# Kernel tuning notes

Measured on AMD Instinct MI355X. Metric: run time of the kernel, lower is better.

The kernel has to match this reference:

```python
import jax, jax.numpy as jnp
import numpy as np

B = 64        # BATCH_SIZE
C_IN = 16
L = 8192
FFT0 = 64
FFT1 = 256
CO = 32       # c_out per fft branch (c_out=64 / 2 ffts)
RATIO = FFT1 // FFT0  # 4
EPS = 1e-5


def setup_inputs() -> dict:
    key = jax.random.key(0)
    ks = jax.random.split(key, 12)
    x = jax.random.normal(ks[0], (B, C_IN, L), jnp.float32)
    bn_gamma = 1.0 + 0.1 * jax.random.normal(ks[1], (2, B), jnp.float32)
    bn_beta = 0.1 * jax.random.normal(ks[2], (2, B), jnp.float32)
    mk_r = 0.1 * jax.random.normal(ks[3], (RATIO, RATIO), jnp.float32)
    mk_i = 0.1 * jax.random.normal(ks[4], (RATIO, RATIO), jnp.float32)
    mb_r = 0.1 * jax.random.normal(ks[5], (RATIO,), jnp.float32)
    mb_i = 0.1 * jax.random.normal(ks[6], (RATIO,), jnp.float32)
    fk0_r = 0.1 * jax.random.normal(ks[7], (FFT0 // 2 + 1, C_IN, CO), jnp.float32)
    fk0_i = 0.1 * jax.random.normal(ks[8], (FFT0 // 2 + 1, C_IN, CO), jnp.float32)
    fk1_r = 0.1 * jax.random.normal(ks[9], (FFT1 // 2 + 1, C_IN, CO), jnp.float32)
    fk1_i = 0.1 * jax.random.normal(ks[10], (FFT1 // 2 + 1, C_IN, CO), jnp.float32)
    pbias = 0.1 * jax.random.normal(ks[11], (2 * CO,), jnp.float32)
    return dict(x=x, bn_gamma=bn_gamma, bn_beta=bn_beta, mk_r=mk_r, mk_i=mk_i,
                mb_r=mb_r, mb_i=mb_i, fk0_r=fk0_r, fk0_i=fk0_i,
                fk1_r=fk1_r, fk1_i=fk1_i, pbias=pbias)


def _stft(x2d, n):
    # torch.stft(center=True, pad_mode='reflect', hop=n_fft, rect window),
    # then keep onesided bins and drop the last frame (as in the module).
    N = x2d.shape[0]
    xp = jnp.pad(x2d, ((0, 0), (n // 2, n // 2)), mode='reflect')
    frames = xp.reshape(N, -1, n)               # (N, T+1, n), hop == n_fft
    spec = jnp.fft.rfft(frames, axis=-1)        # onesided == [:, :, :n//2+1]
    return spec[:, :-1, :]                      # drop last frame -> (N, T, n//2+1)


def _zero_interp(p, ratio, out_f):
    # interleave (ratio-1) zeros along the freq axis, then crop to out_f bins
    b, t, f, c = p.shape
    z = jnp.zeros((b, t, f, ratio - 1, c), p.dtype)
    q = jnp.concatenate([p[:, :, :, None, :], z], axis=3).reshape(b, t, f * ratio, c)
    return q[:, :, :out_f, :]


def _cbn(xc, g, b):
    # BatchNorm2d(BATCH_SIZE) after permute(3,0,1,2): channel dim == batch dim,
    # stats over (c_in, T, F) per batch element; complex mean, |.|^2 variance.
    mu = jnp.mean(xc, axis=(1, 2, 3), keepdims=True)
    d = xc - mu
    var = jnp.mean((d * jnp.conj(d)).real, axis=(1, 2, 3), keepdims=True)
    xh = d / jnp.sqrt(var + EPS)
    return xh * g[:, None, None, None] + b[:, None, None, None]


def _istft(out, n):
    # out: (B, T, F, CO) complex. Mirrors permute/reshape + frame repeat + istft
    # (hop=n_fft, rect window, center=True -> trim n//2 on both ends).
    Bq, T, F, Co = out.shape
    pf = out.transpose(0, 3, 2, 1).reshape(Bq * Co, F, T)
    pf = jnp.concatenate([pf, pf[:, :, :1]], axis=-1)   # append copy of frame 0 -> T+1 frames
    fr = jnp.fft.irfft(pf, n=n, axis=1)                 # (N, n, T+1)
    sig = fr.transpose(0, 2, 1).reshape(Bq * Co, -1)    # overlap-add trivial (hop=n)
    sig = sig[:, n // 2: n // 2 + T * n]                # length L
    return sig.reshape(Bq, Co, -1).transpose(0, 2, 1)   # (B, L, CO)


def _forward(x, bn_gamma, bn_beta, mk_r, mk_i, mb_r, mb_i,
             fk0_r, fk0_i, fk1_r, fk1_i, pbias):
    x2 = x.reshape(B * C_IN, L)

    def spec(n):
        s = _stft(x2, n)                                 # (B*C_IN, T, n//2+1)
        T = s.shape[1]
        return s.reshape(B, C_IN, T, n // 2 + 1).transpose(0, 2, 3, 1)  # (B,T,F,C_IN)

    p0 = spec(FFT0)   # (B, 128, 33, 16)
    p1 = spec(FFT1)   # (B, 32, 129, 16)

    # attention merge across time (small fft -> large fft scale)
    pm = p0.reshape(B, -1, RATIO, FFT0 // 2 + 1, C_IN).transpose(0, 1, 3, 4, 2)  # (B,T1,F0,C,r)
    kc = mk_r + 1j * mk_i
    att = jnp.einsum('btfcr,rs->btfcs', pm, kc) + (mb_r + 1j * mb_i)
    a = jax.nn.softmax(jnp.abs(att), axis=-1)            # real weights (complex(a,0) in torch)
    merged = jnp.sum(pm * a, axis=-1) * float(RATIO)     # (B, T1, F0, C_IN)

    F1 = FFT1 // 2 + 1
    mask01 = _zero_interp(jnp.ones(merged.shape, jnp.float32), RATIO, F1)
    up = _zero_interp(merged, RATIO, F1)

    acc0 = p0                                            # own-scale mask is all ones
    acc1 = mask01 * up + (1.0 - mask01) * p1             # cross-scale + complementary mask

    def head(acc, g, b, fkr, fki, n):
        xbn = _cbn(acc, g, b)
        out = jnp.einsum('btfi,fio->btfo', xbn, fkr + 1j * fki)  # FILTER_FLAG merge
        return _istft(out, n)

    t0 = head(acc0, bn_gamma[0], bn_beta[0], fk0_r, fk0_i, FFT0)  # (B, L, CO)
    t1 = head(acc1, bn_gamma[1], bn_beta[1], fk1_r, fk1_i, FFT1)  # (B, L, CO)

    y = jnp.concatenate([t0, t1], axis=2) + pbias        # + patch_bias.real
    y = jax.nn.relu(y)                                   # ACT_DOMAIN == 'time'
    return y.transpose(0, 2, 1)                          # (B, c_out, L)


def reference(x, bn_gamma, bn_beta, mk_r, mk_i, mb_r, mb_i,
              fk0_r, fk0_i, fk1_r, fk1_i, pbias):
    return _forward(x, bn_gamma, bn_beta, mk_r, mk_i, mb_r, mb_i,
                    fk0_r, fk0_i, fk1_r, fk1_i, pbias)
```

## Files before the change

### kernel.cpp

```cpp
#include <hip/hip_runtime.h>
#include <math.h>

#define BB   64
#define CIN  16
#define LL   8192
#define CO   32
#define TCO  64
constexpr int T0n = 128;
constexpr int T1n = 32;
constexpr int F0n = 33;
constexpr int F1n = 129;

typedef unsigned int   uint32;
typedef unsigned short u16;
typedef __attribute__((ext_vector_type(8))) _Float16 half8;
typedef __attribute__((ext_vector_type(4))) float    f32x4;
typedef __attribute__((ext_vector_type(4))) uint32   u32x4;

__device__ inline int imin(int a, int b) { return a < b ? a : b; }

__device__ inline half8 flip_pm(half8 v) {
    u32x4 u;
    __builtin_memcpy(&u, &v, 16);
    u.y ^= 0x80008000u;
    u.w ^= 0x80008000u;
    half8 r;
    __builtin_memcpy(&r, &u, 16);
    return r;
}

template<int N, int F, int TFR, int NTILES, int KTT, int MT_W, int NT_W,
         int NT_STRIDE, bool MT_SPLIT>
__global__ __launch_bounds__(256)
void stft_mfma_kernel(const float* __restrict__ x,
                      const u16* __restrict__ dhi, const u16* __restrict__ dlo,
                      float* __restrict__ p) {
    constexpr int PADN = N + 8;
    __shared__ __align__(16) u16 Xhi[TFR * PADN];
    __shared__ __align__(16) u16 Xlo[TFR * PADN];
    int bc = blockIdx.x;
    const float* xrow = x + (size_t)bc * LL;

    for (int i = threadIdx.x; i < TFR * N; i += 256) {
        int row = i / N, colk = i % N;
        int gi = i - N / 2;
        gi = gi < 0 ? -gi : gi;
        float v = xrow[gi];
        _Float16 h = (_Float16)v;
        _Float16 l = (_Float16)(v - (float)h);
        Xhi[row * PADN + colk] = *(u16*)&h;
        Xlo[row * PADN + colk] = *(u16*)&l;
    }
    __syncthreads();

    int lane = threadIdx.x & 63, w = threadIdx.x >> 6;
    int col = lane & 15, quad = lane >> 4;
    f32x4 acc[MT_W][NT_W];
    #pragma unroll
    for (int mi = 0; mi < MT_W; ++mi)
        #pragma unroll
        for (int nj = 0; nj < NT_W; ++nj) {
            f32x4 z = {0.f, 0.f, 0.f, 0.f};
            acc[mi][nj] = z;
        }

    for (int kt = 0; kt < KTT; ++kt) {
        half8 ah[MT_W], al[MT_W];
        #pragma unroll
        for (int mi = 0; mi < MT_W; ++mi) {
            int mt = MT_SPLIT ? (w * MT_W + mi) : mi;
            int t  = mt * 16 + col;
            ah[mi] = *(const half8*)&Xhi[t * PADN + kt * 32 + quad * 8];
            al[mi] = *(const half8*)&Xlo[t * PADN + kt * 32 + quad * 8];
        }
        #pragma unroll
        for (int nj = 0; nj < NT_W; ++nj) {
            int nt = MT_SPLIT ? nj : (w + nj * NT_STRIDE);
            if (nt < NTILES) {
                half8 bh = ((const half8*)dhi)[(nt * KTT + kt) * 64 + lane];
                half8 bl = ((const half8*)dlo)[(nt * KTT + kt) * 64 + lane];
                #pragma unroll
                for (int mi = 0; mi < MT_W; ++mi) {
                    acc[mi][nj] = __builtin_amdgcn_mfma_f32_16x16x32_f16(ah[mi], bh, acc[mi][nj], 0, 0, 0);
                    acc[mi][nj] = __builtin_amdgcn_mfma_f32_16x16x32_f16(ah[mi], bl, acc[mi][nj], 0, 0, 0);
                    acc[mi][nj] = __builtin_amdgcn_mfma_f32_16x16x32_f16(al[mi], bh, acc[mi][nj], 0, 0, 0);
                }
            }
        }
    }

    int b = bc / CIN, c = bc % CIN;
    #pragma unroll
    for (int mi = 0; mi < MT_W; ++mi) {
        int mt = MT_SPLIT ? (w * MT_W + mi) : mi;
        #pragma unroll
        for (int nj = 0; nj < NT_W; ++nj) {
            int nt = MT_SPLIT ? nj : (w + nj * NT_STRIDE);
            if (nt < NTILES) {
                int j = nt * 16 + col;
                if (j < 2 * F) {
                    int t0 = mt * 16 + quad * 4;
                    f32x4 a = acc[mi][nj];
                    #pragma unroll
                    for (int r = 0; r < 4; ++r) {
                        p[(((size_t)b * TFR + t0 + r) * CIN + c) * (2 * F) + j] = a[r];
                    }
                }
            }
        }
    }
}

__global__ __launch_bounds__(256)
void init_d_kernel(u16* __restrict__ dhi0, u16* __restrict__ dlo0,
                   u16* __restrict__ dhi1, u16* __restrict__ dlo1) {
    int idx = blockIdx.x * 256 + threadIdx.x;
    constexpr int SZ0 = 5 * 2 * 64 * 8;
    constexpr int SZ1 = 17 * 8 * 64 * 8;
    int N, F, KTT, id; u16 *dh, *dl;
    if (idx < SZ0)            { N = 64;  F = F0n; KTT = 2; dh = dhi0; dl = dlo0; id = idx; }
    else if (idx < SZ0 + SZ1) { N = 256; F = F1n; KTT = 8; dh = dhi1; dl = dlo1; id = idx - SZ0; }
    else return;
    int jj   = id & 7;
    int lane = (id >> 3) & 63;
    int rest = id >> 9;
    int kt   = rest % KTT;
    int nt   = rest / KTT;
    int j = nt * 16 + (lane & 15);
    int k = kt * 32 + (lane >> 4) * 8 + jj;
    float v = 0.f;
    if (j < 2 * F) {
        int f = j >> 1;
        int u = (f * k) % N;
        double th = 6.283185307179586476925286766559 * (double)u / (double)N;
        v = (float)((j & 1) ? -sin(th) : cos(th));
    }
    _Float16 h = (_Float16)v;
    _Float16 l = (_Float16)(v - (float)h);
    dh[id] = *(u16*)&h;
    dl[id] = *(u16*)&l;
}

__global__ __launch_bounds__(256)
void merge_kernel(const float2* __restrict__ p0, float2* __restrict__ p1,
                  const float* __restrict__ mkr, const float* __restrict__ mki,
                  const float* __restrict__ mbr, const float* __restrict__ mbi) {
    int idx = blockIdx.x * 256 + threadIdx.x;
    const int total = BB * T1n * CIN * F0n;
    if (idx >= total) return;
    int f0 = idx % F0n; int r1 = idx / F0n;
    int c  = r1 % CIN;  int r2 = r1 / CIN;
    int t1 = r2 % T1n;  int b  = r2 / T1n;
    float2 pm[4];
    #pragma unroll
    for (int r = 0; r < 4; ++r) {
        int t = t1 * 4 + r;
        pm[r] = p0[(((size_t)b * T0n + t) * CIN + c) * F0n + f0];
    }
    float mag[4], mx = -1e30f;
    #pragma unroll
    for (int s = 0; s < 4; ++s) {
        float atr = mbr[s], ati = mbi[s];
        #pragma unroll
        for (int r = 0; r < 4; ++r) {
            float kr = mkr[r * 4 + s], ki = mki[r * 4 + s];
            atr = fmaf(pm[r].x, kr, atr); atr = fmaf(-pm[r].y, ki, atr);
            ati = fmaf(pm[r].x, ki, ati); ati = fmaf(pm[r].y, kr, ati);
        }
        mag[s] = sqrtf(atr * atr + ati * ati);
        mx = fmaxf(mx, mag[s]);
    }
    float se = 0.f;
    #pragma unroll
    for (int s = 0; s < 4; ++s) { mag[s] = expf(mag[s] - mx); se += mag[s]; }
    float inv = 4.0f / se;
    float mr = 0.f, mi = 0.f;
    #pragma unroll
    for (int r = 0; r < 4; ++r) { mr = fmaf(pm[r].x, mag[r], mr); mi = fmaf(pm[r].y, mag[r], mi); }
    p1[(((size_t)b * T1n + t1) * CIN + c) * F1n + 4 * f0] = make_float2(mr * inv, mi * inv);
}

__global__ __launch_bounds__(256)
void cbn_partial_kernel(const float2* __restrict__ p0, const float2* __restrict__ p1,
                        float4* __restrict__ part) {
    int blk  = blockIdx.x;
    int c8   = blk & 7;
    int b    = (blk >> 3) & 63;
    int head = blk >> 9;
    int Nel  = head ? (T1n * CIN * F1n) : (T0n * CIN * F0n);
    const float2* base = head ? (p1 + (size_t)b * (T1n * CIN * F1n))
                              : (p0 + (size_t)b * (T0n * CIN * F0n));
    int chunk = (Nel + 7) / 8;
    int i0 = c8 * chunk, i1 = imin(i0 + chunk, Nel);
    float sr = 0.f, si = 0.f, s2 = 0.f;
    for (int i = i0 + threadIdx.x; i < i1; i += 256) {
        float2 v = base[i];
        sr += v.x; si += v.y;
        s2 = fmaf(v.x, v.x, s2); s2 = fmaf(v.y, v.y, s2);
    }
    __shared__ float red[3][256];
    red[0][threadIdx.x] = sr; red[1][threadIdx.x] = si; red[2][threadIdx.x] = s2;
    __syncthreads();
    for (int off = 128; off > 0; off >>= 1) {
        if (threadIdx.x < off) {
            red[0][threadIdx.x] += red[0][threadIdx.x + off];
            red[1][threadIdx.x] += red[1][threadIdx.x + off];
            red[2][threadIdx.x] += red[2][threadIdx.x + off];
        }
        __syncthreads();
    }
    if (threadIdx.x == 0)
        part[blk] = make_float4(red[0][0], red[1][0], red[2][0], 0.f);
}

__global__ __launch_bounds__(128)
void cbn_final_kernel(const float4* __restrict__ part,
                      const float* __restrict__ gamma, const float* __restrict__ beta,
                      float4* __restrict__ bn) {
    int hb = threadIdx.x;
    float sr = 0.f, si = 0.f, s2 = 0.f;
    #pragma unroll
    for (int c = 0; c < 8; ++c) {
        float4 v = part[hb * 8 + c];
        sr += v.x; si += v.y; s2 += v.z;
    }
    int head = hb >> 6;
    int Nel  = head ? (T1n * CIN * F1n) : (T0n * CIN * F0n);
    float invN = 1.f / (float)Nel;
    float mur = sr * invN, mui = si * invN;
    float var = s2 * invN - mur * mur - mui * mui;
    float g = gamma[hb] * rsqrtf(var + 1e-5f);
    bn[hb] = make_float4(g, beta[hb] - mur * g, -mui * g, 0.f);
}

__global__ __launch_bounds__(256)
void init_w_kernel(u16* __restrict__ whi0, u16* __restrict__ wlo0,
                   u16* __restrict__ whi1, u16* __restrict__ wlo1) {
    int idx = blockIdx.x * 256 + threadIdx.x;
    constexpr int SZ0 = 2 * 3 * 64 * 8;
    constexpr int SZ1 = 8 * 9 * 64 * 8;
    int N, F, KT, id; u16 *dh, *dl;
    if (idx < SZ0)            { N = 64;  F = F0n; KT = 3; dh = whi0; dl = wlo0; id = idx; }
    else if (idx < SZ0 + SZ1) { N = 256; F = F1n; KT = 9; dh = whi1; dl = wlo1; id = idx - SZ0; }
    else return;
    int j    = id & 7;
    int lane = (id >> 3) & 63;
    int rest = id >> 9;
    int kt   = rest % KT;
    int mt   = rest / KT;
    int m  = mt * 16 + (lane & 15);
    int k2 = kt * 32 + (lane >> 4) * 8 + j;
    float v = 0.f;
    if (k2 < 2 * F) {
        int f = k2 >> 1;
        double scale = (f == 0 || f == F - 1) ? (1024.0 / N) : (2048.0 / N);
        int u = (m * f) % N;
        double th = 6.283185307179586476925286766559 * (double)u / (double)N;
        v = (float)((k2 & 1) ? (-scale * sin(th)) : (scale * cos(th)));
    }
    _Float16 h = (_Float16)v;
    _Float16 l = (_Float16)(v - (float)h);
    dh[id] = *(u16*)&h;
    dl[id] = *(u16*)&l;
}

__global__ __launch_bounds__(256)
void init_fk_kernel(const float* __restrict__ r0, const float* __restrict__ i0,
                    const float* __restrict__ r1, const float* __restrict__ i1,
                    float4* __restrict__ q0, float4* __restrict__ q1,
                    float2* __restrict__ s0, float2* __restrict__ s1) {
    int idx = blockIdx.x * 256 + threadIdx.x;
    constexpr int NQ0 = 8 * F0n * 32;
    constexpr int NQ1 = 8 * F1n * 32;
    constexpr int NS0 = F0n * 32;
    constexpr int NS1 = F1n * 32;
    if (idx < NQ0) {
        int id = idx;
        int c2 = id / (F0n * 32); int rem = id % (F0n * 32);
        int o = rem / F0n, f = rem % F0n;
        int s = (f * CIN + 2 * c2) * CO + o;
        q0[id] = make_float4(r0[s], i0[s], r0[s + CO], i0[s + CO]);
    } else if (idx < NQ0 + NQ1) {
        int id = idx - NQ0;
        int c2 = id / (F1n * 32); int rem = id % (F1n * 32);
        int o = rem / F1n, f = rem % F1n;
        int s = (f * CIN + 2 * c2) * CO + o;
        q1[id] = make_float4(r1[s], i1[s], r1[s + CO], i1[s + CO]);
    } else if (idx < NQ0 + NQ1 + NS0) {
        int id = idx - NQ0 - NQ1;
        int o = id / F0n, f = id % F0n;
        float sr = 0.f, si = 0.f;
        for (int ci = 0; ci < CIN; ++ci) {
            int s = (f * CIN + ci) * CO + o;
            sr += r0[s]; si += i0[s];
        }
        s0[id] = make_float2(sr, si);
    } else if (idx < NQ0 + NQ1 + NS0 + NS1) {
        int id = idx - NQ0 - NQ1 - NS0;
        int o = id / F1n, f = id % F1n;
        float sr = 0.f, si = 0.f;
        for (int ci = 0; ci < CIN; ++ci) {
            int s = (f * CIN + ci) * CO + o;
            sr += r1[s]; si += i1[s];
        }
        s1[id] = make_float2(sr, si);
    }
}

template<int F, int TFR, int CH0, int FCH, int TCH>
__global__ __launch_bounds__(256)
void einsum_kernel(const float2* __restrict__ p, const float4* __restrict__ fkq,
                   const float2* __restrict__ fks, const float4* __restrict__ bn,
                   uint32* __restrict__ Ghi, uint32* __restrict__ Glo) {
    constexpr int FCO  = F * 32;
    constexpr int NFCH = (F + FCH - 1) / FCH;
    constexpr int NTC  = TFR / TCH;
    static_assert(FCH == 8 && TCH * CIN * FCH % 256 == 0, "cfg");
    __shared__ float2 xs[TCH][CIN][FCH];
    int blk  = blockIdx.x;
    int fch  = blk % NFCH;
    int rest = blk / NFCH;
    int tc   = rest % NTC;
    int b    = rest / NTC;
    int t0   = tc * TCH;
    int f0   = fch * FCH;
    int o    = threadIdx.x >> 3;
    int fl   = threadIdx.x & 7;
    int f    = f0 + fl;
    bool valid = f < F;
    int fc = valid ? f : F - 1;
    float4 kk[8];
    #pragma unroll
    for (int c2 = 0; c2 < 8; ++c2) kk[c2] = fkq[c2 * FCO + o * F + fc];
    float2 fv = fks[o * F + fc];
    float4 par = bn[(CH0 ? 1 : 0) * BB + b];
    float base_re = fmaf(par.y, fv.x, -par.z * fv.y);
    float base_im = fmaf(par.y, fv.y,  par.z * fv.x);

    const float2* pb = p + (size_t)(b * TFR + t0) * CIN * F;
    for (int i = threadIdx.x; i < TCH * CIN * FCH; i += 256) {
        int fi = i & 7;
        int r  = i >> 3;
        int ff = f0 + fi;
        ((float2*)xs)[i] = (ff < F) ? pb[(size_t)r * F + ff] : make_float2(0.f, 0.f);
    }
    __syncthreads();
    for (int tp = 0; tp < TCH; ++tp) {
        float re = 0.f, im = 0.f;
        #pragma unroll
        for (int c2 = 0; c2 < 8; ++c2) {
            float2 xa = xs[tp][2 * c2][fl];
            float2 xb = xs[tp][2 * c2 + 1][fl];
            float4 kkc = kk[c2];
            re = fmaf(xa.x, kkc.x, re); re = fmaf(-xa.y, kkc.y, re);
            im = fmaf(xa.x, kkc.y, im); im = fmaf(xa.y, kkc.x, im);
            re = fmaf(xb.x, kkc.z, re); re = fmaf(-xb.y, kkc.w, re);
            im = fmaf(xb.x, kkc.w, im); im = fmaf(xb.y, kkc.z, im);
        }
        if (valid) {
            float res = fmaf(par.x, re, base_re) * 32.f;
            float ims = fmaf(par.x, im, base_im) * 32.f;
            _Float16 rh = (_Float16)res; _Float16 rl = (_Float16)(res - (float)rh);
            _Float16 ih = (_Float16)ims; _Float16 il = (_Float16)(ims - (float)ih);
            size_t d = ((size_t)(b * TFR + t0 + tp) * 32 + o) * F + f;
            Ghi[d] = ((uint32)(*(u16*)&ih) << 16) | (uint32)(*(u16*)&rh);
            Glo[d] = ((uint32)(*(u16*)&il) << 16) | (uint32)(*(u16*)&rl);
        }
    }
}

template<int N, int F, int TFR, int CH0, int KT, int WMT, bool NTSPLIT>
__global__ __launch_bounds__(256)
void irfft_kernel(const uint32* __restrict__ Ghi, const uint32* __restrict__ Glo,
                  const u16* __restrict__ whi, const u16* __restrict__ wlo,
                  const float* __restrict__ pbias, float* __restrict__ out) {
    constexpr int PADW = KT * 16;
    constexpr int LDW  = PADW + 4;
    constexpr int WNT  = NTSPLIT ? 1 : 2;
    __shared__ __align__(16) uint32 buf[2][32 * LDW];
    int t  = blockIdx.x % (TFR + 1);
    int b  = blockIdx.x / (TFR + 1);
    int tf = (t == TFR) ? 0 : t;
    const uint32* sH = Ghi + (size_t)(b * TFR + tf) * 32 * F;
    const uint32* sL = Glo + (size_t)(b * TFR + tf) * 32 * F;
    for (int i = threadIdx.x; i < 32 * F; i += 256) {
        int row = i / F, c = i - row * F;
        buf[0][row * LDW + c] = sH[i];
        buf[1][row * LDW + c] = sL[i];
    }
    for (int i = threadIdx.x; i < 32 * (PADW - F); i += 256) {
        constexpr int cols = PADW - F;
        int row = i / cols, c = i - row * cols;
        buf[0][row * LDW + F + c] = 0;
        buf[1][row * LDW + F + c] = 0;
    }
    __syncthreads();

    int lane = threadIdx.x & 63, w = threadIdx.x >> 6;
    int col = lane & 15, quad = lane >> 4;
    const u16* bufh = (const u16*)&buf[0][0];
    const u16* bufl = (const u16*)&buf[1][0];

    f32x4 accB[WMT][WNT], accD[WMT][WNT];
    #pragma unroll
    for (int mi = 0; mi < WMT; ++mi)
        #pragma unroll
        for (int nj = 0; nj < WNT; ++nj) {
            f32x4 z = {0.f, 0.f, 0.f, 0.f};
            accB[mi][nj] = z; accD[mi][nj] = z;
        }
    for (int kt = 0; kt < KT; ++kt) {
        half8 bh[WNT], bl[WNT], bhm[WNT], blm[WNT];
        #pragma unroll
        for (int nj = 0; nj < WNT; ++nj) {
            int nt = NTSPLIT ? (w & 1) : nj;
            int ro = (nt * 16 + col) * (2 * LDW) + kt * 32 + quad * 8;
            bh[nj]  = *(const half8*)(bufh + ro);
            bl[nj]  = *(const half8*)(bufl + ro);
            bhm[nj] = flip_pm(bh[nj]);
            blm[nj] = flip_pm(bl[nj]);
        }
        #pragma unroll
        for (int mi = 0; mi < WMT; ++mi) {
            int mt = NTSPLIT ? (w >> 1) : (w * WMT + mi);
            half8 ah = ((const half8*)whi)[(mt * KT + kt) * 64 + lane];
            half8 al = ((const half8*)wlo)[(mt * KT + kt) * 64 + lane];
            #pragma unroll
            for (int nj = 0; nj < WNT; ++nj) {
                accB[mi][nj] = __builtin_amdgcn_mfma_f32_16x16x32_f16(ah, bh[nj],  accB[mi][nj], 0, 0, 0);
                accB[mi][nj] = __builtin_amdgcn_mfma_f32_16x16x32_f16(ah, bl[nj],  accB[mi][nj], 0, 0, 0);
                accB[mi][nj] = __builtin_amdgcn_mfma_f32_16x16x32_f16(al, bh[nj],  accB[mi][nj], 0, 0, 0);
                accD[mi][nj] = __builtin_amdgcn_mfma_f32_16x16x32_f16(ah, bhm[nj], accD[mi][nj], 0, 0, 0);
                accD[mi][nj] = __builtin_amdgcn_mfma_f32_16x16x32_f16(ah, blm[nj], accD[mi][nj], 0, 0, 0);
                accD[mi][nj] = __builtin_amdgcn_mfma_f32_16x16x32_f16(al, bhm[nj], accD[mi][nj], 0, 0, 0);
            }
        }
    }
    constexpr float UNSCALE = 1.0f / 32768.0f;
    size_t bb = (size_t)b * TCO;
    #pragma unroll
    for (int mi = 0; mi < WMT; ++mi) {
        int mt = NTSPLIT ? (w >> 1) : (w * WMT + mi);
        #pragma unroll
        for (int hh = 0; hh < 2; ++hh) {
            int m  = mt * 16 + quad * 4 + hh * (N / 2);
            int l0 = t * N + m - N / 2;
            if ((unsigned)l0 < LL) {
                #pragma unroll
                for (int nj = 0; nj < WNT; ++nj) {
                    int nt = NTSPLIT ? (w & 1) : nj;
                    int chn = CH0 + nt * 16 + col;
                    float pb = pbias[chn];
                    f32x4 a = hh ? accD[mi][nj] : accB[mi][nj];
                    float4 v;
                    v.x = fmaxf(fmaf(a[0], UNSCALE, pb), 0.f);
                    v.y = fmaxf(fmaf(a[1], UNSCALE, pb), 0.f);
                    v.z = fmaxf(fmaf(a[2], UNSCALE, pb), 0.f);
                    v.w = fmaxf(fmaf(a[3], UNSCALE, pb), 0.f);
                    *(float4*)(out + (bb + chn) * LL + l0) = v;
                }
            }
        }
    }
}

extern "C" void kernel_launch(void* const* d_in, const int* in_sizes, int n_in,
                              void* d_out, int out_size, void* d_ws, size_t ws_size,
                              hipStream_t stream) {
    const float* x     = (const float*)d_in[0];
    const float* gam   = (const float*)d_in[1];
    const float* bet   = (const float*)d_in[2];
    const float* mkr   = (const float*)d_in[3];
    const float* mki   = (const float*)d_in[4];
    const float* mbr   = (const float*)d_in[5];
    const float* mbi   = (const float*)d_in[6];
    const float* fk0r  = (const float*)d_in[7];
    const float* fk0i  = (const float*)d_in[8];
    const float* fk1r  = (const float*)d_in[9];
    const float* fk1i  = (const float*)d_in[10];
    const float* pbias = (const float*)d_in[11];
    float* out = (float*)d_out;

    float2* p0   = (float2*)d_ws;
    float2* p1   = p0 + (size_t)BB * T0n * CIN * F0n;
    float4* bnp  = (float4*)(p1 + (size_t)BB * T1n * CIN * F1n);
    float4* part = bnp + 2 * BB;
    float4* fkq0 = part + 1024;
    float4* fkq1 = fkq0 + 8 * F0n * 32;
    float2* fks0 = (float2*)(fkq1 + 8 * F1n * 32);
    float2* fks1 = fks0 + F0n * 32;
    uint32* Ghi  = (uint32*)(fks1 + F1n * 32);
    uint32* Glo  = Ghi + (size_t)BB * T0n * 32 * F0n;
    u16*    whi0 = (u16*)(Glo + (size_t)BB * T0n * 32 * F0n);
    u16*    wlo0 = whi0 + 3072;
    u16*    whi1 = wlo0 + 3072;
    u16*    wlo1 = whi1 + 36864;
    u16*    dhi0 = wlo1 + 36864;
    u16*    dlo0 = dhi0 + 5120;
    u16*    dhi1 = dlo0 + 5120;
    u16*    dlo1 = dhi1 + 69632;

    init_w_kernel<<<(3072 + 36864 + 255) / 256, 256, 0, stream>>>(whi0, wlo0, whi1, wlo1);
    init_d_kernel<<<(5120 + 69632 + 255) / 256, 256, 0, stream>>>(dhi0, dlo0, dhi1, dlo1);
    init_fk_kernel<<<(8 * (F0n + F1n) * 32 + (F0n + F1n) * 32 + 255) / 256, 256, 0, stream>>>(
        fk0r, fk0i, fk1r, fk1i, fkq0, fkq1, fks0, fks1);
    stft_mfma_kernel<64, F0n, 128, 5, 2, 2, 5, 1, true><<<BB * CIN, 256, 0, stream>>>(
        x, dhi0, dlo0, (float*)p0);
    stft_mfma_kernel<256, F1n, 32, 17, 8, 2, 5, 4, false><<<BB * CIN, 256, 0, stream>>>(
        x, dhi1, dlo1, (float*)p1);
    merge_kernel<<<(BB * T1n * CIN * F0n) / 256, 256, 0, stream>>>(p0, p1, mkr, mki, mbr, mbi);
    cbn_partial_kernel<<<1024, 256, 0, stream>>>(p0, p1, part);
    cbn_final_kernel<<<1, 128, 0, stream>>>(part, gam, bet, bnp);
    einsum_kernel<F1n, T1n, 32, 8, 16><<<17 * 2 * BB, 256, 0, stream>>>(
        p1, fkq1, fks1, bnp, Ghi, Glo);
    irfft_kernel<256, F1n, T1n, 32, 9, 2, false><<<BB * (T1n + 1), 256, 0, stream>>>(
        Ghi, Glo, whi1, wlo1, pbias, out);
    einsum_kernel<F0n, T0n, 0, 8, 16><<<5 * 8 * BB, 256, 0, stream>>>(
        p0, fkq0, fks0, bnp, Ghi, Glo);
    irfft_kernel<64, F0n, T0n, 0, 3, 1, true><<<BB * (T0n + 1), 256, 0, stream>>>(
        Ghi, Glo, whi0, wlo0, pbias, out);
}
```

Before: 463.2 us.

## Merge per-branch einsum and irfft launches, pad spectra, vectorize STFT staging

The two einsum launches become one kernel and the two irfft launches become one, with the block index choosing the branch. This cuts launch count and lets both branches fill the GPU at the same time. The intermediate spectra are now stored padded to a multiple of 16 columns, with zeros written for the pad. That lets irfft stage them with aligned float4 loads and skip the separate zero-fill loop, at the cost of a larger workspace and some extra writes of padding. The STFT staging loop now reads float4 and writes packed hi/lo halves, with the reflected head handled separately.

```diff
diff --git a/kernel.cpp b/kernel.cpp
--- a/kernel.cpp
+++ b/kernel.cpp
@@ -10,6 +10,8 @@
 constexpr int T1n = 32;
 constexpr int F0n = 33;
 constexpr int F1n = 129;
+constexpr int PW0 = 48;
+constexpr int PW1 = 144;
 
 typedef unsigned int   uint32;
 typedef unsigned short u16;
@@ -18,6 +20,11 @@
 typedef __attribute__((ext_vector_type(4))) uint32   u32x4;
 
 __device__ inline int imin(int a, int b) { return a < b ? a : b; }
+
+__device__ inline uint32 pack2h(float a, float b) {
+    _Float16 ha = (_Float16)a, hb = (_Float16)b;
+    return ((uint32)(*(u16*)&hb) << 16) | (uint32)(*(u16*)&ha);
+}
 
 __device__ inline half8 flip_pm(half8 v) {
     u32x4 u;
@@ -41,15 +48,26 @@
     int bc = blockIdx.x;
     const float* xrow = x + (size_t)bc * LL;
 
-    for (int i = threadIdx.x; i < TFR * N; i += 256) {
-        int row = i / N, colk = i % N;
-        int gi = i - N / 2;
-        gi = gi < 0 ? -gi : gi;
-        float v = xrow[gi];
+    for (int i = threadIdx.x; i < N / 2; i += 256) {
+        float v = xrow[N / 2 - i];
         _Float16 h = (_Float16)v;
+        Xhi[i] = *(u16*)&h;
         _Float16 l = (_Float16)(v - (float)h);
-        Xhi[row * PADN + colk] = *(u16*)&h;
-        Xlo[row * PADN + colk] = *(u16*)&l;
+        Xlo[i] = *(u16*)&l;
+    }
+    for (int i4 = N / 8 + threadIdx.x; i4 < TFR * N / 4; i4 += 256) {
+        int i = 4 * i4;
+        int row = i / N, colk = i - row * N;
+        float4 v = *(const float4*)&xrow[i - N / 2];
+        _Float16 h0 = (_Float16)v.x, h1 = (_Float16)v.y,
+                 h2 = (_Float16)v.z, h3 = (_Float16)v.w;
+        uint2 hv, lv;
+        hv.x = ((uint32)(*(u16*)&h1) << 16) | (uint32)(*(u16*)&h0);
+        hv.y = ((uint32)(*(u16*)&h3) << 16) | (uint32)(*(u16*)&h2);
+        lv.x = pack2h(v.x - (float)h0, v.y - (float)h1);
+        lv.y = pack2h(v.z - (float)h2, v.w - (float)h3);
+        *(uint2*)&Xhi[row * PADN + colk] = hv;
+        *(uint2*)&Xlo[row * PADN + colk] = lv;
     }
     __syncthreads();
 
@@ -307,17 +325,16 @@
     }
 }
 
-template<int F, int TFR, int CH0, int FCH, int TCH>
-__global__ __launch_bounds__(256)
-void einsum_kernel(const float2* __restrict__ p, const float4* __restrict__ fkq,
-                   const float2* __restrict__ fks, const float4* __restrict__ bn,
-                   uint32* __restrict__ Ghi, uint32* __restrict__ Glo) {
+template<int F, int TFR, int CH0, int PADW>
+__device__ __forceinline__ void einsum_body(
+        int blk, float2* xs,
+        const float2* __restrict__ p, const float4* __restrict__ fkq,
+        const float2* __restrict__ fks, const float4* __restrict__ bn,
+        uint32* __restrict__ Ghi, uint32* __restrict__ Glo) {
+    constexpr int FCH = 8, TCH = 16;
     constexpr int FCO  = F * 32;
-    constexpr int NFCH = (F + FCH - 1) / FCH;
+    constexpr int NFCH = PADW / FCH;
     constexpr int NTC  = TFR / TCH;
-    static_assert(FCH == 8 && TCH * CIN * FCH % 256 == 0, "cfg");
-    __shared__ float2 xs[TCH][CIN][FCH];
-    int blk  = blockIdx.x;
     int fch  = blk % NFCH;
     int rest = blk / NFCH;
     int tc   = rest % NTC;
@@ -342,64 +359,80 @@
         int fi = i & 7;
         int r  = i >> 3;
         int ff = f0 + fi;
-        ((float2*)xs)[i] = (ff < F) ? pb[(size_t)r * F + ff] : make_float2(0.f, 0.f);
+        xs[i] = (ff < F) ? pb[(size_t)r * F + ff] : make_float2(0.f, 0.f);
     }
     __syncthreads();
     for (int tp = 0; tp < TCH; ++tp) {
         float re = 0.f, im = 0.f;
         #pragma unroll
         for (int c2 = 0; c2 < 8; ++c2) {
-            float2 xa = xs[tp][2 * c2][fl];
-            float2 xb = xs[tp][2 * c2 + 1][fl];
+            float2 xa = xs[(tp * CIN + 2 * c2) * FCH + fl];
+            float2 xb = xs[(tp * CIN + 2 * c2 + 1) * FCH + fl];
             float4 kkc = kk[c2];
             re = fmaf(xa.x, kkc.x, re); re = fmaf(-xa.y, kkc.y, re);
             im = fmaf(xa.x, kkc.y, im); im = fmaf(xa.y, kkc.x, im);
             re = fmaf(xb.x, kkc.z, re); re = fmaf(-xb.y, kkc.w, re);
             im = fmaf(xb.x, kkc.w, im); im = fmaf(xb.y, kkc.z, im);
         }
+        uint32 hv = 0, lv = 0;
         if (valid) {
             float res = fmaf(par.x, re, base_re) * 32.f;
             float ims = fmaf(par.x, im, base_im) * 32.f;
             _Float16 rh = (_Float16)res; _Float16 rl = (_Float16)(res - (float)rh);
             _Float16 ih = (_Float16)ims; _Float16 il = (_Float16)(ims - (float)ih);
-            size_t d = ((size_t)(b * TFR + t0 + tp) * 32 + o) * F + f;
-            Ghi[d] = ((uint32)(*(u16*)&ih) << 16) | (uint32)(*(u16*)&rh);
-            Glo[d] = ((uint32)(*(u16*)&il) << 16) | (uint32)(*(u16*)&rl);
-        }
-    }
+            hv = ((uint32)(*(u16*)&ih) << 16) | (uint32)(*(u16*)&rh);
+            lv = ((uint32)(*(u16*)&il) << 16) | (uint32)(*(u16*)&rl);
+        }
+        size_t d = ((size_t)(b * TFR + t0 + tp) * 32 + o) * PADW + f;
+        Ghi[d] = hv;
+        Glo[d] = lv;
+    }
+}
+
+__global__ __launch_bounds__(256)
+void einsum_both_kernel(const float2* __restrict__ p1, const float2* __restrict__ p0,
+                        const float4* __restrict__ fkq1, const float2* __restrict__ fks1,
+                        const float4* __restrict__ fkq0, const float2* __restrict__ fks0,
+                        const float4* __restrict__ bn,
+                        uint32* __restrict__ Ghi1, uint32* __restrict__ Glo1,
+                        uint32* __restrict__ Ghi0, uint32* __restrict__ Glo0) {
+    __shared__ float2 xs[16 * CIN * 8];
+    constexpr int NB1 = (PW1 / 8) * (T1n / 16) * BB;
+    int blk = blockIdx.x;
+    if (blk < NB1)
+        einsum_body<F1n, T1n, 32, PW1>(blk, xs, p1, fkq1, fks1, bn, Ghi1, Glo1);
+    else
+        einsum_body<F0n, T0n, 0, PW0>(blk - NB1, xs, p0, fkq0, fks0, bn, Ghi0, Glo0);
 }
 
 template<int N, int F, int TFR, int CH0, int KT, int WMT, bool NTSPLIT>
-__global__ __launch_bounds__(256)
-void irfft_kernel(const uint32* __restrict__ Ghi, const uint32* __restrict__ Glo,
-                  const u16* __restrict__ whi, const u16* __restrict__ wlo,
-                  const float* __restrict__ pbias, float* __restrict__ out) {
+__device__ __forceinline__ void irfft_body(
+        int blk, uint32* bufA,
+        const uint32* __restrict__ Ghi, const uint32* __restrict__ Glo,
+        const u16* __restrict__ whi, const u16* __restrict__ wlo,
+        const float* __restrict__ pbias, float* __restrict__ out) {
     constexpr int PADW = KT * 16;
     constexpr int LDW  = PADW + 4;
+    constexpr int R4   = PADW / 4;
     constexpr int WNT  = NTSPLIT ? 1 : 2;
-    __shared__ __align__(16) uint32 buf[2][32 * LDW];
-    int t  = blockIdx.x % (TFR + 1);
-    int b  = blockIdx.x / (TFR + 1);
+    uint32* bufH = bufA;
+    uint32* bufL = bufA + 32 * LDW;
+    int t  = blk % (TFR + 1);
+    int b  = blk / (TFR + 1);
     int tf = (t == TFR) ? 0 : t;
-    const uint32* sH = Ghi + (size_t)(b * TFR + tf) * 32 * F;
-    const uint32* sL = Glo + (size_t)(b * TFR + tf) * 32 * F;
-    for (int i = threadIdx.x; i < 32 * F; i += 256) {
-        int row = i / F, c = i - row * F;
-        buf[0][row * LDW + c] = sH[i];
-        buf[1][row * LDW + c] = sL[i];
-    }
-    for (int i = threadIdx.x; i < 32 * (PADW - F); i += 256) {
-        constexpr int cols = PADW - F;
-        int row = i / cols, c = i - row * cols;
-        buf[0][row * LDW + F + c] = 0;
-        buf[1][row * LDW + F + c] = 0;
+    const float4* sH = (const float4*)(Ghi + (size_t)(b * TFR + tf) * 32 * PADW);
+    const float4* sL = (const float4*)(Glo + (size_t)(b * TFR + tf) * 32 * PADW);
+    for (int i = threadIdx.x; i < 32 * R4; i += 256) {
+        int row = i / R4, c = i - row * R4;
+        *(float4*)&bufH[row * LDW + 4 * c] = sH[i];
+        *(float4*)&bufL[row * LDW + 4 * c] = sL[i];
     }
     __syncthreads();
 
     int lane = threadIdx.x & 63, w = threadIdx.x >> 6;
     int col = lane & 15, quad = lane >> 4;
-    const u16* bufh = (const u16*)&buf[0][0];
-    const u16* bufl = (const u16*)&buf[1][0];
+    const u16* bufh = (const u16*)bufH;
+    const u16* bufl = (const u16*)bufL;
 
     f32x4 accB[WMT][WNT], accD[WMT][WNT];
     #pragma unroll
@@ -464,6 +497,21 @@
     }
 }
 
+__global__ __launch_bounds__(256)
+void irfft_both_kernel(const uint32* __restrict__ Ghi1, const uint32* __restrict__ Glo1,
+                       const uint32* __restrict__ Ghi0, const uint32* __restrict__ Glo0,
+                       const u16* __restrict__ whi1, const u16* __restrict__ wlo1,
+                       const u16* __restrict__ whi0, const u16* __restrict__ wlo0,
+                       const float* __restrict__ pbias, float* __restrict__ out) {
+    __shared__ __align__(16) uint32 buf[2 * 32 * (PW1 + 4)];
+    constexpr int NB1 = BB * (T1n + 1);
+    int blk = blockIdx.x;
+    if (blk < NB1)
+        irfft_body<256, F1n, T1n, 32, 9, 2, false>(blk, buf, Ghi1, Glo1, whi1, wlo1, pbias, out);
+    else
+        irfft_body<64, F0n, T0n, 0, 3, 1, true>(blk - NB1, buf, Ghi0, Glo0, whi0, wlo0, pbias, out);
+}
+
 extern "C" void kernel_launch(void* const* d_in, const int* in_sizes, int n_in,
                               void* d_out, int out_size, void* d_ws, size_t ws_size,
                               hipStream_t stream) {
@@ -489,9 +537,11 @@
     float4* fkq1 = fkq0 + 8 * F0n * 32;
     float2* fks0 = (float2*)(fkq1 + 8 * F1n * 32);
     float2* fks1 = fks0 + F0n * 32;
-    uint32* Ghi  = (uint32*)(fks1 + F1n * 32);
-    uint32* Glo  = Ghi + (size_t)BB * T0n * 32 * F0n;
-    u16*    whi0 = (u16*)(Glo + (size_t)BB * T0n * 32 * F0n);
+    uint32* Ghi1 = (uint32*)(fks1 + F1n * 32);
+    uint32* Glo1 = Ghi1 + (size_t)BB * T1n * 32 * PW1;
+    uint32* Ghi0 = Glo1 + (size_t)BB * T1n * 32 * PW1;
+    uint32* Glo0 = Ghi0 + (size_t)BB * T0n * 32 * PW0;
+    u16*    whi0 = (u16*)(Glo0 + (size_t)BB * T0n * 32 * PW0);
     u16*    wlo0 = whi0 + 3072;
     u16*    whi1 = wlo0 + 3072;
     u16*    wlo1 = whi1 + 36864;
@@ -511,12 +561,10 @@
     merge_kernel<<<(BB * T1n * CIN * F0n) / 256, 256, 0, stream>>>(p0, p1, mkr, mki, mbr, mbi);
     cbn_partial_kernel<<<1024, 256, 0, stream>>>(p0, p1, part);
     cbn_final_kernel<<<1, 128, 0, stream>>>(part, gam, bet, bnp);
-    einsum_kernel<F1n, T1n, 32, 8, 16><<<17 * 2 * BB, 256, 0, stream>>>(
-        p1, fkq1, fks1, bnp, Ghi, Glo);
-    irfft_kernel<256, F1n, T1n, 32, 9, 2, false><<<BB * (T1n + 1), 256, 0, stream>>>(
-        Ghi, Glo, whi1, wlo1, pbias, out);
-    einsum_kernel<F0n, T0n, 0, 8, 16><<<5 * 8 * BB, 256, 0, stream>>>(
-        p0, fkq0, fks0, bnp, Ghi, Glo);
-    irfft_kernel<64, F0n, T0n, 0, 3, 1, true><<<BB * (T0n + 1), 256, 0, stream>>>(
-        Ghi, Glo, whi0, wlo0, pbias, out);
-}
+    constexpr int NBE = (PW1 / 8) * (T1n / 16) * BB + (PW0 / 8) * (T0n / 16) * BB;
+    einsum_both_kernel<<<NBE, 256, 0, stream>>>(
+        p1, p0, fkq1, fks1, fkq0, fks0, bnp, Ghi1, Glo1, Ghi0, Glo0);
+    constexpr int NBI = BB * (T1n + 1) + BB * (T0n + 1);
+    irfft_both_kernel<<<NBI, 256, 0, stream>>>(
+        Ghi1, Glo1, Ghi0, Glo0, whi1, wlo1, whi0, wlo0, pbias, out);
+}
```

New measurement: 485.6 us. 4.8% more time.
